# Optimization experiments

Hardware: AMD Instinct MI355X
Metric: run time of the kernel (lower is better)

The kernel has to match this reference:

```python
import jax, jax.numpy as jnp
import numpy as np

VOCAB, EMB, HID, OUT = 128, 128, 256, 2
B, T = 128, 2048


def setup_inputs() -> dict:
    key = jax.random.key(0)
    ks = jax.random.split(key, 8)
    s_ih = 1.0 / np.sqrt(HID)
    inp = {
        "x": jax.random.randint(ks[0], (B, T), 0, VOCAB, dtype=jnp.int32),
        "emb": jax.random.normal(ks[1], (VOCAB, EMB), jnp.float32),
        "W_ih": jax.random.uniform(ks[2], (4 * HID, EMB), jnp.float32, -s_ih, s_ih),
        "W_hh": jax.random.uniform(ks[3], (4 * HID, HID), jnp.float32, -s_ih, s_ih),
        "b_ih": jax.random.uniform(ks[4], (4 * HID,), jnp.float32, -s_ih, s_ih),
        "b_hh": jax.random.uniform(ks[5], (4 * HID,), jnp.float32, -s_ih, s_ih),
        "fc_W": jax.random.normal(ks[6], (OUT, HID), jnp.float32) * np.sqrt(6.0 / (HID + OUT)),
        "fc_b": jnp.zeros((OUT,), jnp.float32),
    }
    return inp


def _lstm_last_hidden(xe, W_ih, W_hh, b_ih, b_hh):
    # xe: [B, T, E]. Precompute all input-to-hidden gate projections (batched GEMM).
    Bsz = xe.shape[0]
    H = W_hh.shape[1]
    xg = jnp.einsum('bte,ge->tbg', xe, W_ih) + (b_ih + b_hh)  # [T, B, 4H]

    def step(carry, xt):
        h, c = carry
        g = xt + h @ W_hh.T                 # [B, 4H]
        i, f, gg, o = jnp.split(g, 4, axis=-1)  # PyTorch gate order i,f,g,o
        i = jax.nn.sigmoid(i)
        f = jax.nn.sigmoid(f)
        gg = jnp.tanh(gg)
        o = jax.nn.sigmoid(o)
        c = f * c + i * gg
        h = o * jnp.tanh(c)
        return (h, c), None

    h0 = jnp.zeros((Bsz, H), xe.dtype)
    c0 = jnp.zeros((Bsz, H), xe.dtype)
    (hT, _), _ = jax.lax.scan(step, (h0, c0), xg)
    return hT  # == output[:, -1, :] for a uni-directional LSTM


def reference(x, emb, W_ih, W_hh, b_ih, b_hh, fc_W, fc_b):
    xe = emb[x]                                   # [B, T, E] embedding lookup
    hT = _lstm_last_hidden(xe, W_ih, W_hh, b_ih, b_hh)
    logits = hT @ fc_W.T + fc_b                   # [B, OUT]
    return logits
```

## Files before the change

kernel.cpp:

```cpp
#include <hip/hip_runtime.h>

#define T_LEN 2048
#define HID   256
#define G4    1024
#define EMBD  128
#define VOCAB 128
#define OUTC  2
#define BSUB  4
#define NCHAIN 32
#define CHK   64
#define HSB   288
#define LOG2E 1.44269504088896340736f

typedef int i32x4 __attribute__((ext_vector_type(4)));

__device__ float Pbuf[VOCAB * G4];
__device__ __align__(16) signed char Wqb[G4 * HID];
__device__ float Winv[G4];

__global__ void build_P(const float* __restrict__ emb, const float* __restrict__ W_ih,
                        const float* __restrict__ b_ih, const float* __restrict__ b_hh) {
    const int v = blockIdx.x >> 2;
    const int c = ((blockIdx.x & 3) << 8) + threadIdx.x;
    __shared__ float es[EMBD];
    if (threadIdx.x < EMBD) es[threadIdx.x] = emb[v * EMBD + threadIdx.x];
    __syncthreads();
    const float* wr = W_ih + c * EMBD;
    float acc = 0.f;
    #pragma unroll 8
    for (int e = 0; e < EMBD; ++e) acc += es[e] * wr[e];
    const float ks = ((c >> 8) == 2) ? (-2.f * LOG2E) : (-LOG2E);
    Pbuf[v * G4 + c] = (acc + b_ih[c] + b_hh[c]) * ks;
}

__global__ void quant_W(const float* __restrict__ W_hh) {
    const int row = blockIdx.x;
    const int k   = threadIdx.x;
    __shared__ float red[4];
    const float wv = W_hh[row * HID + k];
    float a = fabsf(wv);
    #pragma unroll
    for (int o = 32; o > 0; o >>= 1) a = fmaxf(a, __shfl_down(a, o, 64));
    if ((k & 63) == 0) red[k >> 6] = a;
    __syncthreads();
    const float m = fmaxf(fmaxf(fmaxf(red[0], red[1]), red[2]), fmaxf(red[3], 1e-30f));
    Wqb[row * HID + k] = (signed char)(int)rintf(wv * (127.f / m));
    const float ks = ((row >> 8) == 2) ? (-2.f * LOG2E) : (-LOG2E);
    if (k == 0) Winv[row] = m * (1.f / (127.f * 127.f)) * ks;
}

__device__ __forceinline__ float sig_p(float p) {
    return __builtin_amdgcn_rcpf(1.f + __builtin_amdgcn_exp2f(p));
}

__global__ __launch_bounds__(512, 2) void lstm_chain(
        const int* __restrict__ x, const float* __restrict__ fc_W,
        const float* __restrict__ fc_b, float* __restrict__ out) {
    __shared__ __align__(16) signed char habuf[2][BSUB * HSB];
    __shared__ int   xch[BSUB * CHK];
    __shared__ float hfin[BSUB * HID];

    const int tid  = threadIdx.x;
    const int w    = tid >> 6;
    const int lane = tid & 63;
    const int l15  = lane & 15;
    const int quad = lane >> 4;
    const int bbase = blockIdx.x * BSUB;
    const int ub    = w * 32;

    i32x4 Bf[2][4][4];
    float winvv[2][4];
    #pragma unroll
    for (int nt = 0; nt < 2; ++nt) {
        #pragma unroll
        for (int g = 0; g < 4; ++g) {
            const int row = g * HID + ub + nt * 16 + l15;
            const signed char* wr = Wqb + (size_t)row * HID;
            winvv[nt][g] = Winv[row];
            #pragma unroll
            for (int kt = 0; kt < 4; ++kt)
                Bf[nt][g][kt] = *(const i32x4*)(wr + kt * 64 + quad * 16);
        }
    }

    for (int i = tid; i < BSUB * HSB; i += 512) habuf[0][i] = 0;

    float cst[2] = {0.f, 0.f};
    float xgv[2][4];

#define GATHER(TT)                                                            \
    {                                                                         \
        const int xv = xch[quad * CHK + (TT)];                                \
        const float* pb = Pbuf + (size_t)xv * G4 + ub + l15;                  \
        _Pragma("unroll")                                                     \
        for (int nt = 0; nt < 2; ++nt)                                        \
            _Pragma("unroll")                                                 \
            for (int g = 0; g < 4; ++g)                                       \
                xgv[nt][g] = pb[g * HID + nt * 16];                           \
    }

#define STEP(T, HB, HN)                                                       \
    {                                                                         \
        const int t  = (T);                                                   \
        const int tt = t & (CHK - 1);                                         \
        if (tt == 0) {                                                        \
            for (int i = tid; i < BSUB * CHK; i += 512)                       \
                xch[i] = x[(bbase + (i >> 6)) * T_LEN + t + (i & (CHK - 1))]; \
            __syncthreads();                                                  \
            GATHER(0);                                                        \
        }                                                                     \
        i32x4 af[4];                                                          \
        _Pragma("unroll")                                                     \
        for (int kt = 0; kt < 4; ++kt)                                        \
            af[kt] = *(const i32x4*)((HB) + (l15 >> 2) * HSB + kt * 64 + quad * 16); \
        i32x4 acc[2][4];                                                      \
        _Pragma("unroll")                                                     \
        for (int nt = 0; nt < 2; ++nt)                                        \
            _Pragma("unroll")                                                 \
            for (int g = 0; g < 4; ++g) {                                     \
                i32x4 z = {0, 0, 0, 0};                                       \
                acc[nt][g] = z;                                               \
            }                                                                 \
        _Pragma("unroll")                                                     \
        for (int kt = 0; kt < 4; ++kt)                                        \
            _Pragma("unroll")                                                 \
            for (int nt = 0; nt < 2; ++nt)                                    \
                _Pragma("unroll")                                             \
                for (int g = 0; g < 4; ++g)                                   \
                    acc[nt][g] = __builtin_amdgcn_mfma_i32_16x16x64_i8(       \
                        af[kt], Bf[nt][g][kt], acc[nt][g], 0, 0, 0);          \
        _Pragma("unroll")                                                     \
        for (int nt = 0; nt < 2; ++nt) {                                      \
            const int col = ub + nt * 16 + l15;                               \
            const float pi = fmaf((float)acc[nt][0][0], winvv[nt][0], xgv[nt][0]); \
            const float pf = fmaf((float)acc[nt][1][0], winvv[nt][1], xgv[nt][1]); \
            const float pg = fmaf((float)acc[nt][2][0], winvv[nt][2], xgv[nt][2]); \
            const float po = fmaf((float)acc[nt][3][0], winvv[nt][3], xgv[nt][3]); \
            const float is = sig_p(pi);                                       \
            const float fs = sig_p(pf);                                       \
            const float gt = fmaf(2.f, sig_p(pg), -1.f);                      \
            const float os = sig_p(po);                                       \
            const float c  = fmaf(fs, cst[nt], is * gt);                      \
            cst[nt] = c;                                                      \
            const float r2    = sig_p(c * (-2.f * LOG2E));                    \
            const float th127 = fmaf(254.f, r2, -127.f);                      \
            const float hq    = th127 * os;                                   \
            (HN)[quad * HSB + col] = (signed char)(int)rintf(hq);             \
            if (t == T_LEN - 1)                                               \
                hfin[quad * HID + col] = hq * (1.f / 127.f);                  \
        }                                                                     \
        if (tt != CHK - 1) GATHER(tt + 1);                                    \
        __syncthreads();                                                      \
    }

    #pragma unroll 1
    for (int t2 = 0; t2 < T_LEN; t2 += 2) {
        STEP(t2,     habuf[0], habuf[1]);
        STEP(t2 + 1, habuf[1], habuf[0]);
    }
#undef STEP
#undef GATHER

    if (tid < BSUB * OUTC) {
        const int b = tid >> 1, o = tid & 1;
        float s = fc_b[o];
        #pragma unroll 8
        for (int j = 0; j < HID; ++j) s += hfin[b * HID + j] * fc_W[o * HID + j];
        out[(bbase + b) * OUTC + o] = s;
    }
}

extern "C" void kernel_launch(void* const* d_in, const int* in_sizes, int n_in,
                              void* d_out, int out_size, void* d_ws, size_t ws_size,
                              hipStream_t stream) {
    const int*   x    = (const int*)  d_in[0];
    const float* emb  = (const float*)d_in[1];
    const float* W_ih = (const float*)d_in[2];
    const float* W_hh = (const float*)d_in[3];
    const float* b_ih = (const float*)d_in[4];
    const float* b_hh = (const float*)d_in[5];
    const float* fc_W = (const float*)d_in[6];
    const float* fc_b = (const float*)d_in[7];
    float* out = (float*)d_out;
    (void)d_ws; (void)ws_size;

    build_P<<<dim3(VOCAB * 4), dim3(256), 0, stream>>>(emb, W_ih, b_ih, b_hh);
    quant_W<<<dim3(G4), dim3(HID), 0, stream>>>(W_hh);
    lstm_chain<<<dim3(NCHAIN), dim3(512), 0, stream>>>(x, fc_W, fc_b, out);
}
```

Before: 1.726 ms.

## Split batch rows into two MFMA groups and overlap gate math with MFMAs

The four batch rows of each workgroup are split into two pairs, each with its own int8 MFMA accumulator chain. The sigmoid/tanh gate math for pair A is interleaved between the MFMAs of pair B, so the transcendental work can overlap the matrix-unit latency on the serial recurrence. Each lane now processes one column tile with a lane-dependent select, instead of computing both nt tiles. This doubles the MFMA count per step, since each half multiplies a padded A tile holding only two real rows, and it raises register pressure from the extra accumulators.

```diff
diff --git a/kernel.cpp b/kernel.cpp
--- a/kernel.cpp
+++ b/kernel.cpp
@@ -6,8 +6,8 @@
 #define EMBD  128
 #define VOCAB 128
 #define OUTC  2
-#define BSUB  4
-#define NCHAIN 32
+#define BROW  4
+#define NWG   32
 #define CHK   64
 #define HSB   288
 #define LOG2E 1.44269504088896340736f
@@ -56,98 +56,118 @@
 __global__ __launch_bounds__(512, 2) void lstm_chain(
         const int* __restrict__ x, const float* __restrict__ fc_W,
         const float* __restrict__ fc_b, float* __restrict__ out) {
-    __shared__ __align__(16) signed char habuf[2][BSUB * HSB];
-    __shared__ int   xch[BSUB * CHK];
-    __shared__ float hfin[BSUB * HID];
+    __shared__ __align__(16) signed char habuf[2][2][2 * HSB];
+    __shared__ int   xch[BROW * CHK];
+    __shared__ float hfin[BROW * HID];
 
     const int tid  = threadIdx.x;
     const int w    = tid >> 6;
     const int lane = tid & 63;
     const int l15  = lane & 15;
     const int quad = lane >> 4;
-    const int bbase = blockIdx.x * BSUB;
+    const int bbase = blockIdx.x * BROW;
     const int ub    = w * 32;
+    const int bq    = quad & 1;
+    const int ntq   = quad >> 1;
+    const int colq  = ub + ntq * 16 + l15;
+    const int arow  = (l15 >> 2) & 1;
 
     i32x4 Bf[2][4][4];
-    float winvv[2][4];
     #pragma unroll
-    for (int nt = 0; nt < 2; ++nt) {
+    for (int nt = 0; nt < 2; ++nt)
         #pragma unroll
         for (int g = 0; g < 4; ++g) {
-            const int row = g * HID + ub + nt * 16 + l15;
-            const signed char* wr = Wqb + (size_t)row * HID;
-            winvv[nt][g] = Winv[row];
+            const signed char* wr = Wqb + (size_t)(g * HID + ub + nt * 16 + l15) * HID;
             #pragma unroll
             for (int kt = 0; kt < 4; ++kt)
                 Bf[nt][g][kt] = *(const i32x4*)(wr + kt * 64 + quad * 16);
         }
-    }
-
-    for (int i = tid; i < BSUB * HSB; i += 512) habuf[0][i] = 0;
+    float winvv[4];
+    #pragma unroll
+    for (int g = 0; g < 4; ++g) winvv[g] = Winv[g * HID + colq];
+
+    for (int i = tid; i < 2 * 2 * HSB; i += 512) ((signed char*)habuf[0])[i] = 0;
 
     float cst[2] = {0.f, 0.f};
-    float xgv[2][4];
+    float xg[2][4];
+    const i32x4 zero4 = {0, 0, 0, 0};
 
 #define GATHER(TT)                                                            \
     {                                                                         \
-        const int xv = xch[quad * CHK + (TT)];                                \
-        const float* pb = Pbuf + (size_t)xv * G4 + ub + l15;                  \
         _Pragma("unroll")                                                     \
-        for (int nt = 0; nt < 2; ++nt)                                        \
+        for (int c = 0; c < 2; ++c) {                                         \
+            const int xv = xch[(c * 2 + bq) * CHK + (TT)];                    \
+            const float* pb = Pbuf + (size_t)xv * G4 + colq;                  \
             _Pragma("unroll")                                                 \
-            for (int g = 0; g < 4; ++g)                                       \
-                xgv[nt][g] = pb[g * HID + nt * 16];                           \
-    }
-
-#define STEP(T, HB, HN)                                                       \
+            for (int g = 0; g < 4; ++g) xg[c][g] = pb[g * HID];               \
+        }                                                                     \
+    }
+
+#define MFMA8(ACC, AF, CSRC)                                                  \
+    _Pragma("unroll")                                                         \
+    for (int nt = 0; nt < 2; ++nt)                                            \
+        _Pragma("unroll")                                                     \
+        for (int g = 0; g < 4; ++g)                                           \
+            ACC[nt][g] = __builtin_amdgcn_mfma_i32_16x16x64_i8(               \
+                (AF), Bf[nt][g][_kt], CSRC, 0, 0, 0);
+
+#define STEP(T, P, PN)                                                        \
     {                                                                         \
         const int t  = (T);                                                   \
         const int tt = t & (CHK - 1);                                         \
         if (tt == 0) {                                                        \
-            for (int i = tid; i < BSUB * CHK; i += 512)                       \
-                xch[i] = x[(bbase + (i >> 6)) * T_LEN + t + (i & (CHK - 1))]; \
+            if (tid < BROW * CHK)                                             \
+                xch[tid] = x[(bbase + (tid >> 6)) * T_LEN + t + (tid & 63)];  \
             __syncthreads();                                                  \
             GATHER(0);                                                        \
         }                                                                     \
-        i32x4 af[4];                                                          \
+        i32x4 afA[4], afB[4];                                                 \
         _Pragma("unroll")                                                     \
-        for (int kt = 0; kt < 4; ++kt)                                        \
-            af[kt] = *(const i32x4*)((HB) + (l15 >> 2) * HSB + kt * 64 + quad * 16); \
-        i32x4 acc[2][4];                                                      \
-        _Pragma("unroll")                                                     \
-        for (int nt = 0; nt < 2; ++nt)                                        \
-            _Pragma("unroll")                                                 \
-            for (int g = 0; g < 4; ++g) {                                     \
-                i32x4 z = {0, 0, 0, 0};                                       \
-                acc[nt][g] = z;                                               \
-            }                                                                 \
-        _Pragma("unroll")                                                     \
-        for (int kt = 0; kt < 4; ++kt)                                        \
-            _Pragma("unroll")                                                 \
-            for (int nt = 0; nt < 2; ++nt)                                    \
-                _Pragma("unroll")                                             \
-                for (int g = 0; g < 4; ++g)                                   \
-                    acc[nt][g] = __builtin_amdgcn_mfma_i32_16x16x64_i8(       \
-                        af[kt], Bf[nt][g][kt], acc[nt][g], 0, 0, 0);          \
-        _Pragma("unroll")                                                     \
-        for (int nt = 0; nt < 2; ++nt) {                                      \
-            const int col = ub + nt * 16 + l15;                               \
-            const float pi = fmaf((float)acc[nt][0][0], winvv[nt][0], xgv[nt][0]); \
-            const float pf = fmaf((float)acc[nt][1][0], winvv[nt][1], xgv[nt][1]); \
-            const float pg = fmaf((float)acc[nt][2][0], winvv[nt][2], xgv[nt][2]); \
-            const float po = fmaf((float)acc[nt][3][0], winvv[nt][3], xgv[nt][3]); \
-            const float is = sig_p(pi);                                       \
-            const float fs = sig_p(pf);                                       \
-            const float gt = fmaf(2.f, sig_p(pg), -1.f);                      \
-            const float os = sig_p(po);                                       \
-            const float c  = fmaf(fs, cst[nt], is * gt);                      \
-            cst[nt] = c;                                                      \
-            const float r2    = sig_p(c * (-2.f * LOG2E));                    \
-            const float th127 = fmaf(254.f, r2, -127.f);                      \
-            const float hq    = th127 * os;                                   \
-            (HN)[quad * HSB + col] = (signed char)(int)rintf(hq);             \
-            if (t == T_LEN - 1)                                               \
-                hfin[quad * HID + col] = hq * (1.f / 127.f);                  \
+        for (int kt = 0; kt < 4; ++kt) {                                      \
+            afA[kt] = *(const i32x4*)(habuf[P][0] + arow * HSB + kt * 64 + quad * 16); \
+            afB[kt] = *(const i32x4*)(habuf[P][1] + arow * HSB + kt * 64 + quad * 16); \
+        }                                                                     \
+        i32x4 accA[2][4], accB[2][4];                                         \
+        { const int _kt = 0; MFMA8(accA, afA[0], zero4) }                     \
+        { const int _kt = 1; MFMA8(accA, afA[1], accA[nt][g]) }               \
+        { const int _kt = 2; MFMA8(accA, afA[2], accA[nt][g]) }               \
+        { const int _kt = 3; MFMA8(accA, afA[3], accA[nt][g]) }               \
+        { const int _kt = 0; MFMA8(accB, afB[0], zero4) }                     \
+        { const int _kt = 1; MFMA8(accB, afB[1], accB[nt][g]) }               \
+                                  \
+        const int aA0 = ntq ? accA[1][0][0] : accA[0][0][0];                  \
+        const int aA1 = ntq ? accA[1][1][0] : accA[0][1][0];                  \
+        const int aA2 = ntq ? accA[1][2][0] : accA[0][2][0];                  \
+        const int aA3 = ntq ? accA[1][3][0] : accA[0][3][0];                  \
+        const float isA = sig_p(fmaf((float)aA0, winvv[0], xg[0][0]));        \
+        const float fsA = sig_p(fmaf((float)aA1, winvv[1], xg[0][1]));        \
+        const float gtA = fmaf(2.f, sig_p(fmaf((float)aA2, winvv[2], xg[0][2])), -1.f); \
+        const float osA = sig_p(fmaf((float)aA3, winvv[3], xg[0][3]));        \
+        { const int _kt = 2; MFMA8(accB, afB[2], accB[nt][g]) }               \
+        { const int _kt = 3; MFMA8(accB, afB[3], accB[nt][g]) }               \
+                                                           \
+        {                                                                     \
+            const float c = fmaf(fsA, cst[0], isA * gtA);                     \
+            cst[0] = c;                                                       \
+            const float hq = fmaf(254.f, sig_p(c * (-2.f * LOG2E)), -127.f) * osA; \
+            habuf[PN][0][bq * HSB + colq] = (signed char)(int)rintf(hq);      \
+            if (t == T_LEN - 1) hfin[bq * HID + colq] = hq * (1.f / 127.f);   \
+        }                                                                     \
+                                    \
+        {                                                                     \
+            const int aB0 = ntq ? accB[1][0][0] : accB[0][0][0];              \
+            const int aB1 = ntq ? accB[1][1][0] : accB[0][1][0];              \
+            const int aB2 = ntq ? accB[1][2][0] : accB[0][2][0];              \
+            const int aB3 = ntq ? accB[1][3][0] : accB[0][3][0];              \
+            const float isB = sig_p(fmaf((float)aB0, winvv[0], xg[1][0]));    \
+            const float fsB = sig_p(fmaf((float)aB1, winvv[1], xg[1][1]));    \
+            const float gtB = fmaf(2.f, sig_p(fmaf((float)aB2, winvv[2], xg[1][2])), -1.f); \
+            const float osB = sig_p(fmaf((float)aB3, winvv[3], xg[1][3]));    \
+            const float c = fmaf(fsB, cst[1], isB * gtB);                     \
+            cst[1] = c;                                                       \
+            const float hq = fmaf(254.f, sig_p(c * (-2.f * LOG2E)), -127.f) * osB; \
+            habuf[PN][1][bq * HSB + colq] = (signed char)(int)rintf(hq);      \
+            if (t == T_LEN - 1) hfin[(2 + bq) * HID + colq] = hq * (1.f / 127.f); \
         }                                                                     \
         if (tt != CHK - 1) GATHER(tt + 1);                                    \
         __syncthreads();                                                      \
@@ -155,13 +175,14 @@
 
     #pragma unroll 1
     for (int t2 = 0; t2 < T_LEN; t2 += 2) {
-        STEP(t2,     habuf[0], habuf[1]);
-        STEP(t2 + 1, habuf[1], habuf[0]);
+        STEP(t2,     0, 1);
+        STEP(t2 + 1, 1, 0);
     }
 #undef STEP
+#undef MFMA8
 #undef GATHER
 
-    if (tid < BSUB * OUTC) {
+    if (tid < BROW * OUTC) {
         const int b = tid >> 1, o = tid & 1;
         float s = fc_b[o];
         #pragma unroll 8
@@ -186,5 +207,5 @@
 
     build_P<<<dim3(VOCAB * 4), dim3(256), 0, stream>>>(emb, W_ih, b_ih, b_hh);
     quant_W<<<dim3(G4), dim3(HID), 0, stream>>>(W_hh);
-    lstm_chain<<<dim3(NCHAIN), dim3(512), 0, stream>>>(x, fc_W, fc_b, out);
-}
+    lstm_chain<<<dim3(NWG), dim3(512), 0, stream>>>(x, fc_W, fc_b, out);
+}
```

After: 2.706 ms. 1.57x slower.
